# Kernel optimization log

Hardware: AMD Instinct MI355X
Metric: run time of the kernel (lower is better)

Reference implementation:

```python
import jax, jax.numpy as jnp
import numpy as np

N = 20000      # nodes
E = 320000     # edges (avg degree 16)
S = 2          # extra feature axis (mean-pooled before fc)
IN = 128       # in_feats
H = 246        # n_hidden (must be 246 to match fc = Linear(246, 1))


def setup_inputs() -> dict:
    key = jax.random.key(0)
    ks = jax.random.split(key, 8)
    feat = jax.random.normal(ks[0], (N, S, IN), jnp.float32)
    src = jax.random.randint(ks[1], (E,), 0, N, jnp.int32)
    dst = jax.random.randint(ks[2], (E,), 0, N, jnp.int32)
    glorot = lambda k, shp, fan: jax.random.normal(k, shp, jnp.float32) / np.sqrt(fan).astype(np.float32)
    return {
        "features": feat,
        "src": src,
        "dst": dst,
        "W0": glorot(ks[3], (IN, H), IN), "b0": jnp.zeros((H,), jnp.float32),
        "W1": glorot(ks[4], (H, H), H),   "b1": jnp.zeros((H,), jnp.float32),
        "W2": glorot(ks[5], (H, H), H),   "b2": jnp.zeros((H,), jnp.float32),
        "fc_w": glorot(ks[6], (H, 1), H), "fc_b": jnp.zeros((1,), jnp.float32),
    }


def reference(features, src, dst, W0, b0, W1, b1, W2, b2, fc_w, fc_b):
    # DGL GraphConv, norm='both': h' = act( D_in^{-1/2} A D_out^{-1/2} h W + b )
    ones = jnp.ones((src.shape[0],), jnp.float32)
    out_deg = jax.ops.segment_sum(ones, src, num_segments=N)
    in_deg = jax.ops.segment_sum(ones, dst, num_segments=N)
    norm_out = jax.lax.rsqrt(jnp.maximum(out_deg, 1.0))[:, None, None]  # [N,1,1]
    norm_in = jax.lax.rsqrt(jnp.maximum(in_deg, 1.0))[:, None, None]

    def graph_conv(h, W, b):
        h = h * norm_out                                      # [N,S,F] scale by src-side norm
        agg = jax.ops.segment_sum(h[src], dst, num_segments=N)  # gather->scatter-add over edges
        agg = agg * norm_in
        return jax.nn.relu(agg @ W + b)

    h = graph_conv(features.astype(jnp.float32), W0, b0)
    # dropout between layers is identity in eval mode
    h = graph_conv(h, W1, b1)
    h = graph_conv(h, W2, b2)
    return h.mean(axis=1) @ fc_w + fc_b  # [N,1]
```

## Files before the change

### kernel.cpp

```cpp
#include <hip/hip_runtime.h>
#include <hip/hip_fp16.h>

#define NN 20000
#define NE 320000
#define SS 2
#define FIN 128
#define FH 246
#define MPAD 40064

typedef _Float16 f16x8 __attribute__((ext_vector_type(8)));
typedef float f32x4 __attribute__((ext_vector_type(4)));

__global__ void degree_kernel(const int* __restrict__ src, const int* __restrict__ dst,
                              int* __restrict__ deg_out, int* __restrict__ deg_in) {
    int e = blockIdx.x * blockDim.x + threadIdx.x;
    if (e < NE) {
        atomicAdd(&deg_out[src[e]], 1);
        atomicAdd(&deg_in[dst[e]], 1);
    }
}

__global__ void alloc_kernel(const int* __restrict__ deg_out, const int* __restrict__ deg_in,
                             float* __restrict__ norm_out, float* __restrict__ norm_in,
                             int* __restrict__ row_start, int* __restrict__ cursor,
                             int* __restrict__ counter) {
    __shared__ int smem[256];
    __shared__ int base_s;
    int tid = threadIdx.x;
    int i = blockIdx.x * 256 + tid;
    int v  = (i < NN) ? deg_in[i] : 0;
    int vp = (v + 3) & ~3;
    smem[tid] = vp;
    __syncthreads();
    for (int off = 1; off < 256; off <<= 1) {
        int t = (tid >= off) ? smem[tid - off] : 0;
        __syncthreads();
        smem[tid] += t;
        __syncthreads();
    }
    int incl = smem[tid];
    if (tid == 0) base_s = atomicAdd(counter, smem[255]);
    __syncthreads();
    if (i < NN) {
        int excl = base_s + incl - vp;
        row_start[i] = excl;
        cursor[i]    = excl;
        norm_out[i] = rsqrtf(fmaxf((float)deg_out[i], 1.0f));
        norm_in[i]  = rsqrtf(fmaxf((float)v, 1.0f));
    }
}

__global__ void scatter_kernel(const int* __restrict__ src, const int* __restrict__ dst,
                               int* __restrict__ cursor, ushort* __restrict__ sorted_src) {
    int e = blockIdx.x * blockDim.x + threadIdx.x;
    if (e < NE) {
        int d = dst[e];
        int pos = atomicAdd(&cursor[d], 1);
        sorted_src[pos] = (ushort)src[e];
    }
}

__global__ void pad_fill(const int* __restrict__ row_start, const int* __restrict__ deg_in,
                         ushort* __restrict__ sorted_src) {
    int n = blockIdx.x * 256 + threadIdx.x;
    if (n < NN) {
        int d = deg_in[n];
        int beg = row_start[n] + d;
        int end = row_start[n] + ((d + 3) & ~3);
        for (int p = beg; p < end; ++p) sorted_src[p] = (ushort)NN;
    }
}

__global__ void convert_w_all(const float* __restrict__ W0, const float* __restrict__ W1,
                              const float* __restrict__ W2,
                              ushort* __restrict__ Wh0, ushort* __restrict__ Wl0,
                              ushort* __restrict__ Wh1, ushort* __restrict__ Wl1,
                              ushort* __restrict__ Wh2, ushort* __restrict__ Wl2) {
    int n = blockIdx.x, k = threadIdx.x;
    const float* W; ushort* Wh; ushort* Wl; int K;
    if (blockIdx.y == 0)      { W = W0; Wh = Wh0; Wl = Wl0; K = FIN; }
    else if (blockIdx.y == 1) { W = W1; Wh = Wh1; Wl = Wl1; K = FH; }
    else                      { W = W2; Wh = Wh2; Wl = Wl2; K = FH; }
    float v = (k < K && n < 246) ? W[k * 246 + n] : 0.f;
    _Float16 h = (_Float16)v;
    _Float16 l = (_Float16)(v - (float)h);
    Wh[n * 256 + k] = *(ushort*)&h;
    Wl[n * 256 + k] = *(ushort*)&l;
}

__global__ void init_out(float* __restrict__ out, const float* __restrict__ fcb,
                         float* __restrict__ norm_out) {
    int i = blockIdx.x * 256 + threadIdx.x;
    if (i < NN) out[i] = fcb[0];
    if (i == 0) norm_out[NN] = 0.f;
}

__global__ void zero_pads(ushort* __restrict__ Ah, ushort* __restrict__ Al) {
    int i = blockIdx.x * 256 + threadIdx.x;
    if (i < 4096) {
        int kt = i >> 9, r = i & 511;
        int m = NN * SS + (r >> 3), j = r & 7;
        size_t o = ((size_t)kt * MPAD + m) * 8 + j;
        ((unsigned long long*)Ah)[o] = 0ull;
        ((unsigned long long*)Al)[o] = 0ull;
    }
}

template<int F4ROW, int NCH, bool NORM>
__global__ void aggregate4(const float* __restrict__ h,
                           const int* __restrict__ row_start,
                           const int* __restrict__ deg_in,
                           const ushort* __restrict__ sorted_src,
                           const float* __restrict__ norm_out,
                           const float* __restrict__ norm_in,
                           ushort* __restrict__ Ah, ushort* __restrict__ Al) {
    constexpr int IHALF = F4ROW / 2;
    int g  = threadIdx.x >> 4;
    int l  = threadIdx.x & 15;
    int cb = blockIdx.x & (NCH - 1);
    int nb = blockIdx.x / NCH;
    int n  = nb * 8 + g;
    if (n >= NN) return;
    int idx = cb * 16 + l;
    const float4* hv = (const float4*)h;
    int beg = row_start[n];
    int end = beg + ((deg_in[n] + 3) & ~3);
    float4 acc = {0.f, 0.f, 0.f, 0.f};
    ushort4 ss;
    if (beg < end) ss = *(const ushort4*)&sorted_src[beg];
    for (int i = beg; i < end; i += 4) {
        ushort4 cur = ss;
        if (i + 4 < end) ss = *(const ushort4*)&sorted_src[i + 4];
        int s0 = cur.x, s1 = cur.y, s2 = cur.z, s3 = cur.w;
        if (NORM) {
            float n0 = norm_out[s0], n1 = norm_out[s1];
            float n2 = norm_out[s2], n3 = norm_out[s3];
            float4 v0 = hv[(size_t)(s0 < NN ? s0 : NN - 1) * F4ROW + idx];
            float4 v1 = hv[(size_t)(s1 < NN ? s1 : NN - 1) * F4ROW + idx];
            float4 v2 = hv[(size_t)(s2 < NN ? s2 : NN - 1) * F4ROW + idx];
            float4 v3 = hv[(size_t)(s3 < NN ? s3 : NN - 1) * F4ROW + idx];
            acc.x += v0.x * n0 + v1.x * n1 + v2.x * n2 + v3.x * n3;
            acc.y += v0.y * n0 + v1.y * n1 + v2.y * n2 + v3.y * n3;
            acc.z += v0.z * n0 + v1.z * n1 + v2.z * n2 + v3.z * n3;
            acc.w += v0.w * n0 + v1.w * n1 + v2.w * n2 + v3.w * n3;
        } else {
            float4 v0 = hv[(size_t)s0 * F4ROW + idx];
            float4 v1 = hv[(size_t)s1 * F4ROW + idx];
            float4 v2 = hv[(size_t)s2 * F4ROW + idx];
            float4 v3 = hv[(size_t)s3 * F4ROW + idx];
            acc.x += v0.x + v1.x + v2.x + v3.x;
            acc.y += v0.y + v1.y + v2.y + v3.y;
            acc.z += v0.z + v1.z + v2.z + v3.z;
            acc.w += v0.w + v1.w + v2.w + v3.w;
        }
    }
    float ni = norm_in[n];
    float v[4] = {acc.x * ni, acc.y * ni, acc.z * ni, acc.w * ni};
    ushort hp[4], lp[4];
#pragma unroll
    for (int j = 0; j < 4; ++j) {
        _Float16 hh = (_Float16)v[j];
        _Float16 ll = (_Float16)(v[j] - (float)hh);
        hp[j] = *(ushort*)&hh;
        lp[j] = *(ushort*)&ll;
    }
    int s  = (idx >= IHALF);
    int ik = idx & (IHALF - 1);
    size_t o = ((size_t)(ik >> 3) * MPAD + n * 2 + s) * 8 + (ik & 7);
    unsigned long long hv64, lv64;
    __builtin_memcpy(&hv64, hp, 8);
    __builtin_memcpy(&lv64, lp, 8);
    __builtin_nontemporal_store(hv64, (unsigned long long*)Ah + o);
    __builtin_nontemporal_store(lv64, (unsigned long long*)Al + o);
}

template<int KP, bool FUSE>
__global__ __launch_bounds__(256) void gemm_split(const ushort* __restrict__ Ah,
                                                  const ushort* __restrict__ Al,
                                                  const ushort* __restrict__ Wh,
                                                  const ushort* __restrict__ Wl,
                                                  const float* __restrict__ b,
                                                  void* __restrict__ outv,
                                                  const float* __restrict__ fcw,
                                                  const float* __restrict__ nrm) {
    constexpr int NT = KP / 32;
    __shared__ __align__(16) _Float16 Bh_s[128][40];
    __shared__ __align__(16) _Float16 Bl_s[128][40];

    int tid  = threadIdx.x;
    int m0   = blockIdx.x * 64;
    int n0   = blockIdx.y * 128;
    int wave = tid >> 6, lane = tid & 63;
    int lr = lane & 15, quad = lane >> 4;
    int wcol = wave * 32;

    f32x4 acc[4][2];
#pragma unroll
    for (int mi = 0; mi < 4; ++mi)
#pragma unroll
        for (int ni = 0; ni < 2; ++ni) acc[mi][ni] = {0.f, 0.f, 0.f, 0.f};

    const uint4* Whv = (const uint4*)Wh;
    const uint4* Wlv = (const uint4*)Wl;

    for (int t0 = 0; t0 < NT; ++t0) {
        f16x8 ah[4], al[4];
#pragma unroll
        for (int mi = 0; mi < 4; ++mi) {
            size_t fh = ((size_t)t0 * MPAD + m0 + mi * 16 + lr) * 32 + quad * 8;
            ah[mi] = *(const f16x8*)(Ah + fh);
            al[mi] = *(const f16x8*)(Al + fh);
        }
#pragma unroll
        for (int it = 0; it < 2; ++it) {
            int f = it * 256 + tid;
            int rn = f >> 2, q = f & 3;
            size_t base = (size_t)(n0 + rn) * 32 + t0 * 4 + q;
            *(uint4*)&Bh_s[rn][q * 8] = Whv[base];
            *(uint4*)&Bl_s[rn][q * 8] = Wlv[base];
        }
        __syncthreads();

        f16x8 bh[2], bl[2];
#pragma unroll
        for (int ni = 0; ni < 2; ++ni) {
            bh[ni] = *(const f16x8*)&Bh_s[wcol + ni * 16 + lr][quad * 8];
            bl[ni] = *(const f16x8*)&Bl_s[wcol + ni * 16 + lr][quad * 8];
        }
#pragma unroll
        for (int mi = 0; mi < 4; ++mi)
#pragma unroll
            for (int ni = 0; ni < 2; ++ni) {
                acc[mi][ni] = __builtin_amdgcn_mfma_f32_16x16x32_f16(ah[mi], bh[ni], acc[mi][ni], 0, 0, 0);
                acc[mi][ni] = __builtin_amdgcn_mfma_f32_16x16x32_f16(al[mi], bh[ni], acc[mi][ni], 0, 0, 0);
                acc[mi][ni] = __builtin_amdgcn_mfma_f32_16x16x32_f16(ah[mi], bl[ni], acc[mi][ni], 0, 0, 0);
            }
        __syncthreads();
    }

    if (FUSE) {
        float* out = (float*)outv;
#pragma unroll
        for (int mi = 0; mi < 4; ++mi) {
#pragma unroll
            for (int i = 0; i < 4; ++i) {
                float p = 0.f;
#pragma unroll
                for (int ni = 0; ni < 2; ++ni) {
                    int c = n0 + wcol + ni * 16 + lr;
                    if (c < 246)
                        p += fmaxf(acc[mi][ni][i] + b[c], 0.f) * fcw[c];
                }
#pragma unroll
                for (int off = 8; off > 0; off >>= 1)
                    p += __shfl_down(p, off, 16);
                int m = m0 + mi * 16 + quad * 4 + i;
                if (lr == 0 && m < NN * SS)
                    atomicAdd(&out[m >> 1], 0.5f * p);
            }
        }
    } else {
        float* outF = (float*)outv;
#pragma unroll
        for (int ni = 0; ni < 2; ++ni) {
            int c = n0 + wcol + ni * 16 + lr;
            float bj = (c < 246) ? b[c] : 0.f;
#pragma unroll
            for (int mi = 0; mi < 4; ++mi)
#pragma unroll
                for (int i = 0; i < 4; ++i) {
                    int m = m0 + mi * 16 + quad * 4 + i;
                    if (m < NN * SS) {
                        float no = nrm[m >> 1];
                        outF[(size_t)m * 256 + c] = fmaxf(acc[mi][ni][i] + bj, 0.f) * no;
                    }
                }
        }
    }
}

extern "C" void kernel_launch(void* const* d_in, const int* in_sizes, int n_in,
                              void* d_out, int out_size, void* d_ws, size_t ws_size,
                              hipStream_t stream) {
    const float* feat = (const float*)d_in[0];
    const int*   src  = (const int*)d_in[1];
    const int*   dst  = (const int*)d_in[2];
    const float* W0   = (const float*)d_in[3];
    const float* b0   = (const float*)d_in[4];
    const float* W1   = (const float*)d_in[5];
    const float* b1   = (const float*)d_in[6];
    const float* W2   = (const float*)d_in[7];
    const float* b2   = (const float*)d_in[8];
    const float* fcw  = (const float*)d_in[9];
    const float* fcb  = (const float*)d_in[10];
    float* out = (float*)d_out;

    char* ws = (char*)d_ws;
    size_t off = 0;
    auto alloc = [&](size_t bytes) {
        void* p = ws + off;
        off = (off + bytes + 255) & ~(size_t)255;
        return p;
    };
    int*    deg_out_i = (int*)alloc((2 * NN + 64) * sizeof(int));
    int*    deg_in_i  = deg_out_i + NN;
    int*    counter   = deg_out_i + 2 * NN;
    int*    row_start = (int*)alloc(NN * sizeof(int));
    int*    cursor    = (int*)alloc(NN * sizeof(int));
    ushort* sorted    = (ushort*)alloc((NE + 3 * NN + 16) * sizeof(ushort));
    float*  norm_out  = (float*)alloc((NN + 1) * sizeof(float));
    float*  norm_in   = (float*)alloc(NN * sizeof(float));
    ushort* Wh0 = (ushort*)alloc(256 * 256 * sizeof(ushort));
    ushort* Wl0 = (ushort*)alloc(256 * 256 * sizeof(ushort));
    ushort* Wh1 = (ushort*)alloc(256 * 256 * sizeof(ushort));
    ushort* Wl1 = (ushort*)alloc(256 * 256 * sizeof(ushort));
    ushort* Wh2 = (ushort*)alloc(256 * 256 * sizeof(ushort));
    ushort* Wl2 = (ushort*)alloc(256 * 256 * sizeof(ushort));
    ushort* Ahb = (ushort*)alloc((size_t)MPAD * 256 * sizeof(ushort));
    ushort* Alb = (ushort*)alloc((size_t)MPAD * 256 * sizeof(ushort));
    float*  bufH = (float*)alloc(((size_t)NN * SS * 256 + 512) * sizeof(float));

    hipMemsetAsync(deg_out_i, 0, (2 * NN + 1) * sizeof(int), stream);
    hipMemsetAsync(bufH + (size_t)NN * 512, 0, 512 * sizeof(float), stream);

    degree_kernel<<<(NE + 255) / 256, 256, 0, stream>>>(src, dst, deg_out_i, deg_in_i);
    alloc_kernel<<<(NN + 255) / 256, 256, 0, stream>>>(deg_out_i, deg_in_i, norm_out, norm_in,
                                                       row_start, cursor, counter);
    pad_fill<<<(NN + 255) / 256, 256, 0, stream>>>(row_start, deg_in_i, sorted);
    scatter_kernel<<<(NE + 255) / 256, 256, 0, stream>>>(src, dst, cursor, sorted);

    convert_w_all<<<dim3(256, 3), 256, 0, stream>>>(W0, W1, W2, Wh0, Wl0, Wh1, Wl1, Wh2, Wl2);
    init_out<<<(NN + 255) / 256, 256, 0, stream>>>(out, fcb, norm_out);
    zero_pads<<<16, 256, 0, stream>>>(Ahb, Alb);

    const int NB8 = (NN + 7) / 8;
    dim3 ggrid(MPAD / 64, 2);

    aggregate4<64, 4, true><<<NB8 * 4, 128, 0, stream>>>(feat, row_start, deg_in_i, sorted,
                                                         norm_out, norm_in, Ahb, Alb);
    gemm_split<FIN, false><<<ggrid, 256, 0, stream>>>(Ahb, Alb, Wh0, Wl0, b0, bufH, fcw, norm_out);

    aggregate4<128, 8, false><<<NB8 * 8, 128, 0, stream>>>(bufH, row_start, deg_in_i, sorted,
                                                           norm_out, norm_in, Ahb, Alb);
    gemm_split<256, false><<<ggrid, 256, 0, stream>>>(Ahb, Alb, Wh1, Wl1, b1, bufH, fcw, norm_out);

    aggregate4<128, 8, false><<<NB8 * 8, 128, 0, stream>>>(bufH, row_start, deg_in_i, sorted,
                                                           norm_out, norm_in, Ahb, Alb);
    gemm_split<256, true><<<ggrid, 256, 0, stream>>>(Ahb, Alb, Wh2, Wl2, b2, out, fcw, norm_out);
}
```

Baseline: 396.0 us.

## Keep GEMM weight fragments in registers via MFMA-ordered prepacked layout

```diff
diff --git a/kernel.cpp b/kernel.cpp
--- a/kernel.cpp
+++ b/kernel.cpp
@@ -84,8 +84,10 @@
     float v = (k < K && n < 246) ? W[k * 246 + n] : 0.f;
     _Float16 h = (_Float16)v;
     _Float16 l = (_Float16)(v - (float)h);
-    Wh[n * 256 + k] = *(ushort*)&h;
-    Wl[n * 256 + k] = *(ushort*)&l;
+    int c16 = n >> 4, lr = n & 15, kt = k >> 5, quad = (k >> 3) & 3, j = k & 7;
+    int off = ((c16 * 8 + kt) * 64 + quad * 16 + lr) * 8 + j;
+    Wh[off] = *(ushort*)&h;
+    Wl[off] = *(ushort*)&l;
 }
 
 __global__ void init_out(float* __restrict__ out, const float* __restrict__ fcb,
@@ -175,24 +177,32 @@
 }
 
 template<int KP, bool FUSE>
-__global__ __launch_bounds__(256) void gemm_split(const ushort* __restrict__ Ah,
-                                                  const ushort* __restrict__ Al,
-                                                  const ushort* __restrict__ Wh,
-                                                  const ushort* __restrict__ Wl,
-                                                  const float* __restrict__ b,
-                                                  void* __restrict__ outv,
-                                                  const float* __restrict__ fcw,
-                                                  const float* __restrict__ nrm) {
+__global__ __launch_bounds__(256, 1) void gemm_breg(const ushort* __restrict__ Ah,
+                                                    const ushort* __restrict__ Al,
+                                                    const ushort* __restrict__ Whp,
+                                                    const ushort* __restrict__ Wlp,
+                                                    const float* __restrict__ b,
+                                                    void* __restrict__ outv,
+                                                    const float* __restrict__ fcw,
+                                                    const float* __restrict__ nrm) {
     constexpr int NT = KP / 32;
-    __shared__ __align__(16) _Float16 Bh_s[128][40];
-    __shared__ __align__(16) _Float16 Bl_s[128][40];
-
     int tid  = threadIdx.x;
     int m0   = blockIdx.x * 64;
     int n0   = blockIdx.y * 128;
     int wave = tid >> 6, lane = tid & 63;
     int lr = lane & 15, quad = lane >> 4;
     int wcol = wave * 32;
+    int c0 = (n0 + wcol) >> 4;
+
+    f16x8 bh[2][NT], bl[2][NT];
+#pragma unroll
+    for (int ni = 0; ni < 2; ++ni)
+#pragma unroll
+        for (int kt = 0; kt < NT; ++kt) {
+            size_t o = ((size_t)((c0 + ni) * 8 + kt) * 64 + lane) * 8;
+            bh[ni][kt] = *(const f16x8*)(Whp + o);
+            bl[ni][kt] = *(const f16x8*)(Wlp + o);
+        }
 
     f32x4 acc[4][2];
 #pragma unroll
@@ -200,9 +210,7 @@
 #pragma unroll
         for (int ni = 0; ni < 2; ++ni) acc[mi][ni] = {0.f, 0.f, 0.f, 0.f};
 
-    const uint4* Whv = (const uint4*)Wh;
-    const uint4* Wlv = (const uint4*)Wl;
-
+#pragma unroll
     for (int t0 = 0; t0 < NT; ++t0) {
         f16x8 ah[4], al[4];
 #pragma unroll
@@ -212,30 +220,13 @@
             al[mi] = *(const f16x8*)(Al + fh);
         }
 #pragma unroll
-        for (int it = 0; it < 2; ++it) {
-            int f = it * 256 + tid;
-            int rn = f >> 2, q = f & 3;
-            size_t base = (size_t)(n0 + rn) * 32 + t0 * 4 + q;
-            *(uint4*)&Bh_s[rn][q * 8] = Whv[base];
-            *(uint4*)&Bl_s[rn][q * 8] = Wlv[base];
-        }
-        __syncthreads();
-
-        f16x8 bh[2], bl[2];
-#pragma unroll
-        for (int ni = 0; ni < 2; ++ni) {
-            bh[ni] = *(const f16x8*)&Bh_s[wcol + ni * 16 + lr][quad * 8];
-            bl[ni] = *(const f16x8*)&Bl_s[wcol + ni * 16 + lr][quad * 8];
-        }
-#pragma unroll
         for (int mi = 0; mi < 4; ++mi)
 #pragma unroll
             for (int ni = 0; ni < 2; ++ni) {
-                acc[mi][ni] = __builtin_amdgcn_mfma_f32_16x16x32_f16(ah[mi], bh[ni], acc[mi][ni], 0, 0, 0);
-                acc[mi][ni] = __builtin_amdgcn_mfma_f32_16x16x32_f16(al[mi], bh[ni], acc[mi][ni], 0, 0, 0);
-                acc[mi][ni] = __builtin_amdgcn_mfma_f32_16x16x32_f16(ah[mi], bl[ni], acc[mi][ni], 0, 0, 0);
+                acc[mi][ni] = __builtin_amdgcn_mfma_f32_16x16x32_f16(ah[mi], bh[ni][t0], acc[mi][ni], 0, 0, 0);
+                acc[mi][ni] = __builtin_amdgcn_mfma_f32_16x16x32_f16(al[mi], bh[ni][t0], acc[mi][ni], 0, 0, 0);
+                acc[mi][ni] = __builtin_amdgcn_mfma_f32_16x16x32_f16(ah[mi], bl[ni][t0], acc[mi][ni], 0, 0, 0);
             }
-        __syncthreads();
     }
 
     if (FUSE) {
@@ -338,13 +329,13 @@
 
     aggregate4<64, 4, true><<<NB8 * 4, 128, 0, stream>>>(feat, row_start, deg_in_i, sorted,
                                                          norm_out, norm_in, Ahb, Alb);
-    gemm_split<FIN, false><<<ggrid, 256, 0, stream>>>(Ahb, Alb, Wh0, Wl0, b0, bufH, fcw, norm_out);
+    gemm_breg<FIN, false><<<ggrid, 256, 0, stream>>>(Ahb, Alb, Wh0, Wl0, b0, bufH, fcw, norm_out);
 
     aggregate4<128, 8, false><<<NB8 * 8, 128, 0, stream>>>(bufH, row_start, deg_in_i, sorted,
                                                            norm_out, norm_in, Ahb, Alb);
-    gemm_split<256, false><<<ggrid, 256, 0, stream>>>(Ahb, Alb, Wh1, Wl1, b1, bufH, fcw, norm_out);
+    gemm_breg<256, false><<<ggrid, 256, 0, stream>>>(Ahb, Alb, Wh1, Wl1, b1, bufH, fcw, norm_out);
 
     aggregate4<128, 8, false><<<NB8 * 8, 128, 0, stream>>>(bufH, row_start, deg_in_i, sorted,
                                                            norm_out, norm_in, Ahb, Alb);
-    gemm_split<256, true><<<ggrid, 256, 0, stream>>>(Ahb, Alb, Wh2, Wl2, b2, out, fcw, norm_out);
-}
+    gemm_breg<256, true><<<ggrid, 256, 0, stream>>>(Ahb, Alb, Wh2, Wl2, b2, out, fcw, norm_out);
+}
```

Result: no change. 388.7 us (-1.8%).
